# Optimization experiments

Measured on AMD Instinct MI355X. Metric: run time of the kernel, lower is better.

The kernel has to match this reference:

```python
import jax, jax.numpy as jnp
import numpy as np

H, W, C, UP = 32, 32, 1024, 2  # num_patch=(32,32), embed_dim=1024, upsample_rate=2


def setup_inputs() -> dict:
    key = jax.random.key(0)
    k1, k2 = jax.random.split(key)
    x = jax.random.normal(k1, (32, H * W, C), dtype=jnp.float32)
    # keras Conv2D 1x1 kernel (1,1,Cin,Cout) squeezed to (Cin, Cout); Cin = Cout = C//UP
    w = jax.random.normal(k2, (C // UP, C // UP), dtype=jnp.float32) * 0.02
    return {"x": x, "w": w}


def reference(x, w):
    B, L, Cin = x.shape
    assert L == H * W and Cin == C
    xg = x.reshape(B, H, W, C)
    x0 = xg[..., : C // UP]        # [B,H,W,C/2]
    x1 = xg[..., C // UP:]         # [B,H,W,C/2]
    # Row-wise interleave: output rows alternate x0[i], x1[i] -> [B, 2H, W, C/2]
    xi = jnp.stack([x0, x1], axis=2).reshape(B, 2 * H, W, C // UP)
    # 1x1 conv (no bias) == per-pixel linear projection C/2 -> C/2
    y = jnp.einsum('bhwc,cd->bhwd', xi, w)
    # return_vector=True: tokens [B, 2L, C//2]
    return y.reshape(B, L * UP, C // 2)
```

## Files before the change

### kernel.cpp

```cpp
#include <hip/hip_runtime.h>
#include <hip/hip_bf16.h>
#include <stdint.h>

typedef __attribute__((ext_vector_type(4))) float f32x4;
typedef __attribute__((ext_vector_type(16))) float f32x16;
typedef __attribute__((ext_vector_type(8))) short bf16x8;
typedef __attribute__((ext_vector_type(4))) uint32_t u32x4;

#define KD 512
#define ND 512

__device__ __forceinline__ uint32_t pk_bf16(float lo, float hi) {
  uint32_t ulo = __float_as_uint(lo) + 0x8000u;
  uint32_t uhi = __float_as_uint(hi) + 0x8000u;
  return __builtin_amdgcn_perm(uhi, ulo, 0x07060302u);
}

__global__ void wt_kernel(const float* __restrict__ w, uint16_t* __restrict__ wt) {
  __shared__ float tile[32][33];
  const int bx = blockIdx.x, by = blockIdx.y;
  const int tx = threadIdx.x, ty = threadIdx.y;
#pragma unroll
  for (int i = 0; i < 32; i += 8)
    tile[ty + i][tx] = w[(bx * 32 + ty + i) * ND + by * 32 + tx];
  __syncthreads();
#pragma unroll
  for (int i = 0; i < 32; i += 8) {
    uint32_t u = __float_as_uint(tile[tx][ty + i]);
    uint32_t r = (u + 0x7FFFu + ((u >> 16) & 1u)) >> 16;
    wt[(by * 32 + ty + i) * KD + bx * 32 + tx] = (uint16_t)r;
  }
}

__global__ __launch_bounds__(256, 2) void gemm_kernel(
    const float* __restrict__ x, const uint16_t* __restrict__ wt,
    float* __restrict__ out) {
  __shared__ uint16_t As[64 * 512];

  const int tid = threadIdx.x;
  const int lane = tid & 63;
  const int l31 = lane & 31, hi = lane >> 5;
  const int wid = tid >> 6;
  const int m0 = blockIdx.x * 64;

  {
    const int r = tid >> 2;
    const int c0 = tid & 3;
    const int aRow = m0 + ((r & 31) << 1) + (r >> 5);
    const char* src = (const char*)x + (size_t)aRow * (KD * 4) + c0 * 32;
    char* dst = (char*)As + r * 1024;
    const int rx = (r & 7) << 1;
#pragma unroll 4
    for (int i = 0; i < 16; ++i) {
      const int c = c0 + i * 4;
      f32x4 lo = *(const f32x4*)(src + i * 128);
      f32x4 h4 = *(const f32x4*)(src + i * 128 + 16);
      u32x4 p = {pk_bf16(lo.x, lo.y), pk_bf16(lo.z, lo.w),
                 pk_bf16(h4.x, h4.y), pk_bf16(h4.z, h4.w)};
      *(u32x4*)(dst + (c ^ rx) * 16) = p;
    }
  }
  __syncthreads();

  const char* wb = (const char*)wt;
  uint32_t wOff[4];
#pragma unroll
  for (int tn = 0; tn < 4; ++tn)
    wOff[tn] = (uint32_t)(wid * 128 + tn * 32 + l31) * (KD * 2) + hi * 16;

  uint32_t aBase[2], aXor[2];
#pragma unroll
  for (int tm = 0; tm < 2; ++tm) {
    const int u = tm * 32 + l31;
    aBase[tm] = u * 1024;
    aXor[tm] = (u & 7) << 1;
  }

  f32x16 acc[2][4];
#pragma unroll
  for (int tm = 0; tm < 2; ++tm)
#pragma unroll
    for (int tn = 0; tn < 4; ++tn)
#pragma unroll
      for (int e = 0; e < 16; ++e) acc[tm][tn][e] = 0.f;

  bf16x8 wf[2][4];
#pragma unroll
  for (int tn = 0; tn < 4; ++tn)
    wf[0][tn] = *(const bf16x8*)(wb + wOff[tn]);

#pragma unroll 4
  for (int ks = 0; ks < 32; ++ks) {
    const int p = ks & 1;
    if (ks + 1 < 32) {
#pragma unroll
      for (int tn = 0; tn < 4; ++tn)
        wf[p ^ 1][tn] = *(const bf16x8*)(wb + wOff[tn] + (ks + 1) * 32);
    }
    bf16x8 af[2];
#pragma unroll
    for (int tm = 0; tm < 2; ++tm) {
      const uint32_t s = (uint32_t)(2 * ks + hi) ^ aXor[tm];
      af[tm] = *(const bf16x8*)((const char*)As + aBase[tm] + s * 16);
    }
#pragma unroll
    for (int tm = 0; tm < 2; ++tm)
#pragma unroll
      for (int tn = 0; tn < 4; ++tn)
        acc[tm][tn] = __builtin_amdgcn_mfma_f32_32x32x16_bf16(
            wf[p][tn], af[tm], acc[tm][tn], 0, 0, 0);
  }

#pragma unroll
  for (int tm = 0; tm < 2; ++tm) {
    float* op = out + (size_t)(m0 + tm * 32 + l31) * ND + wid * 128;
#pragma unroll
    for (int tn = 0; tn < 4; ++tn) {
#pragma unroll
      for (int q = 0; q < 4; ++q) {
        f32x4 v = {acc[tm][tn][q * 4 + 0], acc[tm][tn][q * 4 + 1],
                   acc[tm][tn][q * 4 + 2], acc[tm][tn][q * 4 + 3]};
        *(f32x4*)(op + tn * 32 + q * 8 + hi * 4) = v;
      }
    }
  }
}

extern "C" void kernel_launch(void* const* d_in, const int* in_sizes, int n_in,
                              void* d_out, int out_size, void* d_ws, size_t ws_size,
                              hipStream_t stream) {
  const float* x = (const float*)d_in[0];
  const float* w = (const float*)d_in[1];
  float* out = (float*)d_out;
  uint16_t* wt = (uint16_t*)d_ws;

  wt_kernel<<<dim3(16, 16), dim3(32, 8), 0, stream>>>(w, wt);
  gemm_kernel<<<dim3(1024), dim3(256), 0, stream>>>(x, wt, out);
}
```

Before: 284.9 us.

## Restructure GEMM loop to hold full-K weight column in registers per column group

Replaces the double-buffered K loop over a 2x4 accumulator tile with an outer loop over four column groups. Each group loads a full-K slice of 32 bf16x8 weight fragments into registers, then runs two single-accumulator MFMA chains over the two row groups and writes the output right away. This cuts accumulator register pressure and issues weight loads in bulk rather than interleaved, but each wave now reads its A fragments from LDS four times and serializes on one accumulator per chain. The A-staging loop is also unrolled 8 instead of 4.

```diff
diff --git a/kernel.cpp b/kernel.cpp
--- a/kernel.cpp
+++ b/kernel.cpp
@@ -50,7 +50,7 @@
     const char* src = (const char*)x + (size_t)aRow * (KD * 4) + c0 * 32;
     char* dst = (char*)As + r * 1024;
     const int rx = (r & 7) << 1;
-#pragma unroll 4
+#pragma unroll 8
     for (int i = 0; i < 16; ++i) {
       const int c = c0 + i * 4;
       f32x4 lo = *(const f32x4*)(src + i * 128);
@@ -63,64 +63,40 @@
   __syncthreads();
 
   const char* wb = (const char*)wt;
-  uint32_t wOff[4];
-#pragma unroll
-  for (int tn = 0; tn < 4; ++tn)
-    wOff[tn] = (uint32_t)(wid * 128 + tn * 32 + l31) * (KD * 2) + hi * 16;
-
   uint32_t aBase[2], aXor[2];
 #pragma unroll
-  for (int tm = 0; tm < 2; ++tm) {
-    const int u = tm * 32 + l31;
-    aBase[tm] = u * 1024;
-    aXor[tm] = (u & 7) << 1;
+  for (int rg = 0; rg < 2; ++rg) {
+    const int u = rg * 32 + l31;
+    aBase[rg] = u * 1024;
+    aXor[rg] = (u & 7) << 1;
   }
 
-  f32x16 acc[2][4];
+#pragma unroll 1
+  for (int cg = 0; cg < 4; ++cg) {
+    const uint32_t col = (uint32_t)(cg * 128 + wid * 32 + l31);
+    const char* wp = wb + col * (KD * 2) + hi * 16;
+    bf16x8 wreg[32];
 #pragma unroll
-  for (int tm = 0; tm < 2; ++tm)
-#pragma unroll
-    for (int tn = 0; tn < 4; ++tn)
-#pragma unroll
-      for (int e = 0; e < 16; ++e) acc[tm][tn][e] = 0.f;
-
-  bf16x8 wf[2][4];
-#pragma unroll
-  for (int tn = 0; tn < 4; ++tn)
-    wf[0][tn] = *(const bf16x8*)(wb + wOff[tn]);
-
-#pragma unroll 4
-  for (int ks = 0; ks < 32; ++ks) {
-    const int p = ks & 1;
-    if (ks + 1 < 32) {
-#pragma unroll
-      for (int tn = 0; tn < 4; ++tn)
-        wf[p ^ 1][tn] = *(const bf16x8*)(wb + wOff[tn] + (ks + 1) * 32);
-    }
-    bf16x8 af[2];
-#pragma unroll
-    for (int tm = 0; tm < 2; ++tm) {
-      const uint32_t s = (uint32_t)(2 * ks + hi) ^ aXor[tm];
-      af[tm] = *(const bf16x8*)((const char*)As + aBase[tm] + s * 16);
-    }
-#pragma unroll
-    for (int tm = 0; tm < 2; ++tm)
-#pragma unroll
-      for (int tn = 0; tn < 4; ++tn)
-        acc[tm][tn] = __builtin_amdgcn_mfma_f32_32x32x16_bf16(
-            wf[p][tn], af[tm], acc[tm][tn], 0, 0, 0);
-  }
+    for (int ks = 0; ks < 32; ++ks)
+      wreg[ks] = *(const bf16x8*)(wp + ks * 32);
 
 #pragma unroll
-  for (int tm = 0; tm < 2; ++tm) {
-    float* op = out + (size_t)(m0 + tm * 32 + l31) * ND + wid * 128;
+    for (int rg = 0; rg < 2; ++rg) {
+      f32x16 acc;
 #pragma unroll
-    for (int tn = 0; tn < 4; ++tn) {
+      for (int e = 0; e < 16; ++e) acc[e] = 0.f;
+#pragma unroll
+      for (int ks = 0; ks < 32; ++ks) {
+        const uint32_t s = (uint32_t)(2 * ks + hi) ^ aXor[rg];
+        bf16x8 af = *(const bf16x8*)((const char*)As + aBase[rg] + s * 16);
+        acc = __builtin_amdgcn_mfma_f32_32x32x16_bf16(wreg[ks], af, acc, 0, 0, 0);
+      }
+      float* op = out + (size_t)(m0 + rg * 32 + l31) * ND + cg * 128 + wid * 32;
 #pragma unroll
       for (int q = 0; q < 4; ++q) {
-        f32x4 v = {acc[tm][tn][q * 4 + 0], acc[tm][tn][q * 4 + 1],
-                   acc[tm][tn][q * 4 + 2], acc[tm][tn][q * 4 + 3]};
-        *(f32x4*)(op + tn * 32 + q * 8 + hi * 4) = v;
+        f32x4 v = {acc[q * 4 + 0], acc[q * 4 + 1],
+                   acc[q * 4 + 2], acc[q * 4 + 3]};
+        *(f32x4*)(op + q * 8 + hi * 4) = v;
       }
     }
   }
```

Result: slower. 318.2 us (+11.7%).
